# Kernel optimization log

Measured on AMD Instinct MI355X. Metric: run time of the kernel, lower is better.

The kernel has to match this reference:

```python
import jax, jax.numpy as jnp
import numpy as np
from jax import lax

_EPS = 1e-6
N_POINTS = 2048


def quat_to_rot(q):
    # q = (x, y, z, w), same convention as quaternion_to_rotation_matrix_torch
    # (its analytic Jacobians dR/dq in the kernel match this unnormalized form)
    x, y, z, w = q[0], q[1], q[2], q[3]
    return jnp.stack([
        jnp.stack([1 - 2 * (y * y + z * z), 2 * (x * y - z * w), 2 * (x * z + y * w)]),
        jnp.stack([2 * (x * y + z * w), 1 - 2 * (x * x + z * z), 2 * (y * z - x * w)]),
        jnp.stack([2 * (x * z - y * w), 2 * (y * z + x * w), 1 - 2 * (x * x + y * y)]),
    ])


def setup_inputs() -> dict:
    key = jax.random.key(0)
    ks = jax.random.split(key, 8)
    H, W = 512, 512
    # points in front of camera, projecting inside the image
    z = jax.random.uniform(ks[0], (N_POINTS, 1), minval=2.0, maxval=6.0)
    xy_dir = jax.random.uniform(ks[1], (N_POINTS, 2), minval=-0.45, maxval=0.45)
    pointcloud = jnp.concatenate([xy_dir * z, z], axis=1)  # [N,3]
    point_color = jax.random.uniform(ks[2], (N_POINTS, 3))
    point_alpha = jax.random.uniform(ks[3], (N_POINTS,), minval=0.1, maxval=0.9)
    # conic = inverse 2x2 covariance in pixel space, stored (a, b, c):
    ac = jax.random.uniform(ks[4], (N_POINTS, 2), minval=0.02, maxval=0.10)
    b = jax.random.uniform(ks[5], (N_POINTS, 1), minval=-0.01, maxval=0.01)
    point_conic = jnp.concatenate([ac[:, :1], b, ac[:, 1:]], axis=1)  # [N,3]
    # near-identity camera pose (x,y,z,w quaternion)
    q = jnp.array([0.01, -0.02, 0.015, 1.0], dtype=jnp.float32)
    q_pointcloud_camera = q / jnp.linalg.norm(q)
    t_pointcloud_camera = 0.05 * jax.random.normal(ks[6], (3,), dtype=jnp.float32)
    fx = fy = 500.0
    camera_intrinsics = jnp.array([[fx, 0.0, W / 2.0], [0.0, fy, H / 2.0], [0.0, 0.0, 1.0]], dtype=jnp.float32)
    return {
        "pointcloud": pointcloud.astype(jnp.float32),
        "point_color": point_color.astype(jnp.float32),
        "point_alpha": point_alpha.astype(jnp.float32),
        "point_conic": point_conic.astype(jnp.float32),
        "q_pointcloud_camera": q_pointcloud_camera,
        "t_pointcloud_camera": t_pointcloud_camera,
        "camera_intrinsics": camera_intrinsics,
        "camera_height": H,
        "camera_width": W,
    }


def _rasterize(pointcloud, point_color, point_alpha, point_conic, q, t, K, H, W):
    R = quat_to_rot(q)
    p_cam = pointcloud @ R.T + t  # [N,3] camera-frame positions
    depth = p_cam[:, 2]
    proj = p_cam @ K.T
    uv = proj[:, :2] / (depth[:, None] + _EPS)  # [N,2] pixel coords
    # depth sort (front-to-back), matching the sorted per-tile traversal
    order = jnp.argsort(depth)
    uv_s = uv[order]
    conic_s = point_conic[order]
    col_s = point_color[order]
    a_s = point_alpha[order]
    d_s = depth[order]

    px = jnp.arange(W, dtype=jnp.float32) + 0.5  # pixel centers, as in kernel
    py = jnp.arange(H, dtype=jnp.float32) + 0.5

    def step(carry, xs):
        T, rgb, dacc = carry
        uv_i, conic_i, col_i, a_i, d_i = xs
        dx = px[None, :] - uv_i[0]  # [1,W] -> broadcast [H,W]
        dy = py[:, None] - uv_i[1]  # [H,1]
        power = -0.5 * (conic_i[0] * dx * dx + 2.0 * conic_i[1] * dx * dy + conic_i[2] * dy * dy)
        g = jnp.exp(jnp.minimum(power, 0.0))  # gaussian density in [0,1]
        prod = g * a_i
        alpha = jnp.where(prod >= 1.0 / 255.0, jnp.minimum(prod, 0.99), 0.0)
        w = T * alpha
        rgb = rgb + w[..., None] * col_i
        dacc = dacc + w * d_i
        T = T * (1.0 - alpha)
        return (T, rgb, dacc), None

    carry0 = (jnp.ones((H, W), jnp.float32), jnp.zeros((H, W, 3), jnp.float32), jnp.zeros((H, W), jnp.float32))
    (T, rgb, dacc), _ = lax.scan(step, carry0, (uv_s, conic_s, col_s, a_s, d_s))
    # [H,W,5] = rgb, rasterized_depth, accumulated_alpha
    return jnp.concatenate([rgb, dacc[..., None], (1.0 - T)[..., None]], axis=-1)


def reference(pointcloud, point_color, point_alpha, point_conic, q_pointcloud_camera, t_pointcloud_camera, camera_intrinsics, camera_height, camera_width):
    return _rasterize(pointcloud, point_color, point_alpha, point_conic,
                      q_pointcloud_camera, t_pointcloud_camera, camera_intrinsics,
                      camera_height, camera_width)
```

## Files before the change

### kernel.cpp

```cpp
#include <hip/hip_runtime.h>
#include <math.h>

#define NPTS 2048
#define IMG_W 512
#define IMG_H 512
#define TILE 16
#define CAP 384
#define RSTRIDE 12

__global__ __launch_bounds__(256) void gs_fused(
    const float* __restrict__ pc,
    const float* __restrict__ col,
    const float* __restrict__ alp,
    const float* __restrict__ con,
    const float* __restrict__ q,
    const float* __restrict__ t,
    const float* __restrict__ K,
    float* __restrict__ out) {
  __shared__ float s_pts[CAP * RSTRIDE];
  __shared__ float2 s_do[CAP];
  __shared__ int s_cnt[32];

  int tid = threadIdx.x;
  int lane = tid & 63, wave = tid >> 6;
  int tilex = (blockIdx.x % (IMG_W / TILE)) * TILE;
  int tiley = (blockIdx.x / (IMG_W / TILE)) * TILE;
  int lx = tid % TILE, ly = tid / TILE;
  float px = tilex + lx + 0.5f, py = tiley + ly + 0.5f;
  float tx0 = tilex + 0.5f, tx1 = tilex + TILE - 0.5f;
  float ty0 = tiley + 0.5f, ty1 = tiley + TILE - 0.5f;

  float qx = q[0], qy = q[1], qz = q[2], qw = q[3];
  float r00 = 1.f - 2.f * (qy * qy + qz * qz), r01 = 2.f * (qx * qy - qz * qw),
        r02 = 2.f * (qx * qz + qy * qw);
  float r10 = 2.f * (qx * qy + qz * qw), r11 = 1.f - 2.f * (qx * qx + qz * qz),
        r12 = 2.f * (qy * qz - qx * qw);
  float r20 = 2.f * (qx * qz - qy * qw), r21 = 2.f * (qy * qz + qx * qw),
        r22 = 1.f - 2.f * (qx * qx + qy * qy);
  float t0 = t[0], t1 = t[1], t2 = t[2];
  float fx = K[0], cx = K[2], fy = K[4], cy = K[5];

#define PROJ(i, ux, uy, Z)                              \
  float ux, uy, Z;                                      \
  {                                                     \
    float x = pc[3 * (i)], y = pc[3 * (i) + 1],         \
          z = pc[3 * (i) + 2];                          \
    Z = r20 * x + r21 * y + r22 * z + t2;               \
    float X = r00 * x + r01 * y + r02 * z + t0;         \
    float Y = r10 * x + r11 * y + r12 * z + t1;         \
    float inv = 1.0f / (Z + 1e-6f);                     \
    ux = (fx * X + cx * Z) * inv;                       \
    uy = (fy * Y + cy * Z) * inv;                       \
  }

  unsigned pmask = 0;
  int miw[8];
#pragma unroll
  for (int c = 0; c < 8; c++) {
    int i = c * 256 + tid;
    PROJ(i, ux, uy, Z);
    float A = con[3 * i], B = con[3 * i + 1], C = con[3 * i + 2];
    float a = alp[i];
    float th = 2.0f * __logf(255.0f * a);
    float absB = fabsf(B);
    float dxm = fmaxf(0.0f, fmaxf(tx0 - ux, ux - tx1));
    float dym = fmaxf(0.0f, fmaxf(ty0 - uy, uy - ty1));
    float bound =
        fmaxf(A - absB, 0.0f) * dxm * dxm + fmaxf(C - absB, 0.0f) * dym * dym;
    bool pred = bound <= th + 1e-3f;
    unsigned long long m = __ballot(pred);
    miw[c] = __popcll(m & ((1ull << lane) - 1ull));
    if (lane == 0) s_cnt[c * 4 + wave] = (int)__popcll(m);
    pmask |= (unsigned)pred << c;
  }
  __syncthreads();

  int start[8], total;
  {
    int run = 0;
#pragma unroll
    for (int c = 0; c < 8; c++) {
      int s0 = s_cnt[c * 4 + 0], s1 = s_cnt[c * 4 + 1];
      int s2 = s_cnt[c * 4 + 2], s3 = s_cnt[c * 4 + 3];
      start[c] = run + (wave > 0 ? s0 : 0) + (wave > 1 ? s1 : 0) +
                 (wave > 2 ? s2 : 0);
      run += s0 + s1 + s2 + s3;
    }
    total = run;
  }

  float T = 1.0f, accr = 0.f, accg = 0.f, accb = 0.f, accd = 0.f;

#define COMPOSITE(w0, w1, w2)                                              \
  {                                                                        \
    float dx = px - w0.x, dy = py - w0.y;                                  \
    float pw =                                                             \
        -0.5f * (w0.z * dx * dx + 2.0f * w0.w * dx * dy + w1.x * dy * dy); \
    float gg = __expf(fminf(pw, 0.0f));                                    \
    float prod = gg * w1.y;                                                \
    if (prod >= (1.0f / 255.0f)) {                                         \
      float al = fminf(prod, 0.99f);                                       \
      float w = T * al;                                                    \
      accr += w * w2.x;                                                    \
      accg += w * w2.y;                                                    \
      accb += w * w2.z;                                                    \
      accd += w * w1.z;                                                    \
      T *= (1.0f - al);                                                    \
    }                                                                      \
  }

  if (total <= CAP) {
#pragma unroll
    for (int c = 0; c < 8; c++) {
      if ((pmask >> c) & 1) {
        int i = c * 256 + tid;
        PROJ(i, ux, uy, Z);
        float a = alp[i];
        int slot = start[c] + miw[c];
        float4* d = (float4*)(s_pts + (size_t)slot * RSTRIDE);
        d[0] = {ux, uy, con[3 * i], con[3 * i + 1]};
        d[1] = {con[3 * i + 2], a, Z, (float)i};
        d[2] = {col[3 * i], col[3 * i + 1], col[3 * i + 2], 0.0f};
        s_do[slot] = {Z, (float)i};
      }
    }
    __syncthreads();

    int k1 = tid, k2 = tid + 256;
    bool h1 = k1 < total, h2 = k2 < total;
    float2 d1 = h1 ? s_do[k1] : make_float2(1e30f, 1e30f);
    float2 d2 = h2 ? s_do[k2] : make_float2(1e30f, 1e30f);
    int r1 = 0, r2 = 0;
    for (int j = 0; j < total; j++) {
      float2 v = s_do[j];
      r1 += (v.x < d1.x) || (v.x == d1.x && v.y < d1.y);
      r2 += (v.x < d2.x) || (v.x == d2.x && v.y < d2.y);
    }
    float4 a1, b1, c1, a2, b2, c2;
    if (h1) {
      const float4* s = (const float4*)(s_pts + (size_t)k1 * RSTRIDE);
      a1 = s[0]; b1 = s[1]; c1 = s[2];
    }
    if (h2) {
      const float4* s = (const float4*)(s_pts + (size_t)k2 * RSTRIDE);
      a2 = s[0]; b2 = s[1]; c2 = s[2];
    }
    __syncthreads();
    if (h1) {
      float4* d = (float4*)(s_pts + (size_t)r1 * RSTRIDE);
      d[0] = a1; d[1] = b1; d[2] = c1;
    }
    if (h2) {
      float4* d = (float4*)(s_pts + (size_t)r2 * RSTRIDE);
      d[0] = a2; d[1] = b2; d[2] = c2;
    }
    __syncthreads();

    for (int k = 0; k < total; k++) {
      const float4* p4 = (const float4*)(s_pts + (size_t)k * RSTRIDE);
      float4 w0 = p4[0], w1 = p4[1], w2 = p4[2];
      COMPOSITE(w0, w1, w2);
      if (T < 1e-4f) break;
    }
  } else {
    float dep[8];
#pragma unroll
    for (int c = 0; c < 8; c++) {
      int i = c * 256 + tid;
      float x = pc[3 * i], y = pc[3 * i + 1], z = pc[3 * i + 2];
      dep[c] = r20 * x + r21 * y + r22 * z + t2;
    }
    unsigned live = pmask;
    float* s_rd = s_pts;
    int* s_ro = (int*)(s_pts + 256);
    float* s_rec = s_pts + 512;
    while (1) {
      float bd = 1e30f;
      int bo = 0x7fffffff;
#pragma unroll
      for (int c = 0; c < 8; c++) {
        if ((live >> c) & 1) {
          int o = c * 256 + tid;
          if (dep[c] < bd || (dep[c] == bd && o < bo)) { bd = dep[c]; bo = o; }
        }
      }
      s_rd[tid] = bd;
      s_ro[tid] = bo;
      __syncthreads();
      float wd = 1e30f;
      int wo = 0x7fffffff;
      for (int j = 0; j < 256; j++) {
        float d = s_rd[j];
        int o = s_ro[j];
        if (d < wd || (d == wd && o < wo)) { wd = d; wo = o; }
      }
      __syncthreads();
      if (wo == 0x7fffffff) break;
      if (tid == (wo & 255)) {
        int i = wo;
        PROJ(i, ux, uy, Z);
        float a = alp[i];
        float4* d = (float4*)s_rec;
        d[0] = {ux, uy, con[3 * i], con[3 * i + 1]};
        d[1] = {con[3 * i + 2], a, Z, (float)i};
        d[2] = {col[3 * i], col[3 * i + 1], col[3 * i + 2], 0.0f};
        live &= ~(1u << (wo >> 8));
      }
      __syncthreads();
      float4 w0 = ((float4*)s_rec)[0], w1 = ((float4*)s_rec)[1],
             w2 = ((float4*)s_rec)[2];
      COMPOSITE(w0, w1, w2);
    }
  }
#undef COMPOSITE
#undef PROJ

  int o = ((tiley + ly) * IMG_W + (tilex + lx)) * 5;
  out[o + 0] = accr;
  out[o + 1] = accg;
  out[o + 2] = accb;
  out[o + 3] = accd;
  out[o + 4] = 1.0f - T;
}

extern "C" void kernel_launch(void* const* d_in, const int* in_sizes, int n_in,
                              void* d_out, int out_size, void* d_ws,
                              size_t ws_size, hipStream_t stream) {
  const float* pc = (const float*)d_in[0];
  const float* col = (const float*)d_in[1];
  const float* alp = (const float*)d_in[2];
  const float* con = (const float*)d_in[3];
  const float* q = (const float*)d_in[4];
  const float* t = (const float*)d_in[5];
  const float* K = (const float*)d_in[6];
  float* out = (float*)d_out;

  gs_fused<<<(IMG_H / TILE) * (IMG_W / TILE), 256, 0, stream>>>(
      pc, col, alp, con, q, t, K, out);
}
```

Measured before the change: 20.80 us.

## Use 32x16 tiles with 512 threads and sort by index permutation

Grows each block to a 32x16 pixel tile with 512 threads, so there are half as many blocks and each loads the point list once for twice as many pixels. Sorting now ranks packed 64-bit (depth, index) keys, one per thread, and writes a permutation array instead of scattering the 48-byte records. Compositing reads records indirectly through that permutation. The early exit when transmittance drops below 1e-4 is removed, so every pixel walks the whole list, which can add compositing work.

Result: faster. 18.38 us (-11.6%).

```diff
diff --git a/kernel.cpp b/kernel.cpp
--- a/kernel.cpp
+++ b/kernel.cpp
@@ -4,11 +4,16 @@
 #define NPTS 2048
 #define IMG_W 512
 #define IMG_H 512
-#define TILE 16
-#define CAP 384
+#define RW 32
+#define RH 16
+#define NBX (IMG_W / RW)
+#define NBY (IMG_H / RH)
+#define NTHREADS (RW * RH)
+#define NCHUNK (NPTS / NTHREADS)
+#define CAP 512
 #define RSTRIDE 12
 
-__global__ __launch_bounds__(256) void gs_fused(
+__global__ __launch_bounds__(NTHREADS) void gs_fused(
     const float* __restrict__ pc,
     const float* __restrict__ col,
     const float* __restrict__ alp,
@@ -18,17 +23,18 @@
     const float* __restrict__ K,
     float* __restrict__ out) {
   __shared__ float s_pts[CAP * RSTRIDE];
-  __shared__ float2 s_do[CAP];
-  __shared__ int s_cnt[32];
+  __shared__ unsigned long long s_key[CAP];
+  __shared__ int s_order[CAP];
+  __shared__ int s_cnt[NCHUNK * 8];
 
   int tid = threadIdx.x;
   int lane = tid & 63, wave = tid >> 6;
-  int tilex = (blockIdx.x % (IMG_W / TILE)) * TILE;
-  int tiley = (blockIdx.x / (IMG_W / TILE)) * TILE;
-  int lx = tid % TILE, ly = tid / TILE;
-  float px = tilex + lx + 0.5f, py = tiley + ly + 0.5f;
-  float tx0 = tilex + 0.5f, tx1 = tilex + TILE - 0.5f;
-  float ty0 = tiley + 0.5f, ty1 = tiley + TILE - 0.5f;
+  int rx = (blockIdx.x % NBX) * RW;
+  int ry = (blockIdx.x / NBX) * RH;
+  int lx = tid % RW, ly = tid / RW;
+  float px = rx + lx + 0.5f, py = ry + ly + 0.5f;
+  float tx0 = rx + 0.5f, tx1 = rx + RW - 0.5f;
+  float ty0 = ry + 0.5f, ty1 = ry + RH - 0.5f;
 
   float qx = q[0], qy = q[1], qz = q[2], qw = q[3];
   float r00 = 1.f - 2.f * (qy * qy + qz * qz), r01 = 2.f * (qx * qy - qz * qw),
@@ -40,24 +46,24 @@
   float t0 = t[0], t1 = t[1], t2 = t[2];
   float fx = K[0], cx = K[2], fy = K[4], cy = K[5];
 
-#define PROJ(i, ux, uy, Z)                              \
-  float ux, uy, Z;                                      \
-  {                                                     \
-    float x = pc[3 * (i)], y = pc[3 * (i) + 1],         \
-          z = pc[3 * (i) + 2];                          \
-    Z = r20 * x + r21 * y + r22 * z + t2;               \
-    float X = r00 * x + r01 * y + r02 * z + t0;         \
-    float Y = r10 * x + r11 * y + r12 * z + t1;         \
-    float inv = 1.0f / (Z + 1e-6f);                     \
-    ux = (fx * X + cx * Z) * inv;                       \
-    uy = (fy * Y + cy * Z) * inv;                       \
+#define PROJ(i, ux, uy, Z)                      \
+  float ux, uy, Z;                              \
+  {                                             \
+    float x = pc[3 * (i)], y = pc[3 * (i) + 1], \
+          z = pc[3 * (i) + 2];                  \
+    Z = r20 * x + r21 * y + r22 * z + t2;       \
+    float X = r00 * x + r01 * y + r02 * z + t0; \
+    float Y = r10 * x + r11 * y + r12 * z + t1; \
+    float inv = 1.0f / (Z + 1e-6f);             \
+    ux = (fx * X + cx * Z) * inv;               \
+    uy = (fy * Y + cy * Z) * inv;               \
   }
 
   unsigned pmask = 0;
-  int miw[8];
-#pragma unroll
-  for (int c = 0; c < 8; c++) {
-    int i = c * 256 + tid;
+  int miw[NCHUNK];
+#pragma unroll
+  for (int c = 0; c < NCHUNK; c++) {
+    int i = c * NTHREADS + tid;
     PROJ(i, ux, uy, Z);
     float A = con[3 * i], B = con[3 * i + 1], C = con[3 * i + 2];
     float a = alp[i];
@@ -70,21 +76,25 @@
     bool pred = bound <= th + 1e-3f;
     unsigned long long m = __ballot(pred);
     miw[c] = __popcll(m & ((1ull << lane) - 1ull));
-    if (lane == 0) s_cnt[c * 4 + wave] = (int)__popcll(m);
+    if (lane == 0) s_cnt[c * 8 + wave] = (int)__popcll(m);
     pmask |= (unsigned)pred << c;
   }
   __syncthreads();
 
-  int start[8], total;
+  int start[NCHUNK], total;
   {
     int run = 0;
 #pragma unroll
-    for (int c = 0; c < 8; c++) {
-      int s0 = s_cnt[c * 4 + 0], s1 = s_cnt[c * 4 + 1];
-      int s2 = s_cnt[c * 4 + 2], s3 = s_cnt[c * 4 + 3];
-      start[c] = run + (wave > 0 ? s0 : 0) + (wave > 1 ? s1 : 0) +
-                 (wave > 2 ? s2 : 0);
-      run += s0 + s1 + s2 + s3;
+    for (int c = 0; c < NCHUNK; c++) {
+      int woff = 0, ct = 0;
+#pragma unroll
+      for (int w = 0; w < 8; w++) {
+        int v = s_cnt[c * 8 + w];
+        woff += (w < wave) ? v : 0;
+        ct += v;
+      }
+      start[c] = run + woff;
+      run += ct;
     }
     total = run;
   }
@@ -111,76 +121,56 @@
 
   if (total <= CAP) {
 #pragma unroll
-    for (int c = 0; c < 8; c++) {
+    for (int c = 0; c < NCHUNK; c++) {
       if ((pmask >> c) & 1) {
-        int i = c * 256 + tid;
+        int i = c * NTHREADS + tid;
         PROJ(i, ux, uy, Z);
         float a = alp[i];
+        float th = 2.0f * __logf(255.0f * a);
         int slot = start[c] + miw[c];
         float4* d = (float4*)(s_pts + (size_t)slot * RSTRIDE);
         d[0] = {ux, uy, con[3 * i], con[3 * i + 1]};
-        d[1] = {con[3 * i + 2], a, Z, (float)i};
+        d[1] = {con[3 * i + 2], a, Z, th};
         d[2] = {col[3 * i], col[3 * i + 1], col[3 * i + 2], 0.0f};
-        s_do[slot] = {Z, (float)i};
+        s_key[slot] =
+            ((unsigned long long)__float_as_uint(Z) << 32) | (unsigned)i;
       }
     }
     __syncthreads();
 
-    int k1 = tid, k2 = tid + 256;
-    bool h1 = k1 < total, h2 = k2 < total;
-    float2 d1 = h1 ? s_do[k1] : make_float2(1e30f, 1e30f);
-    float2 d2 = h2 ? s_do[k2] : make_float2(1e30f, 1e30f);
-    int r1 = 0, r2 = 0;
-    for (int j = 0; j < total; j++) {
-      float2 v = s_do[j];
-      r1 += (v.x < d1.x) || (v.x == d1.x && v.y < d1.y);
-      r2 += (v.x < d2.x) || (v.x == d2.x && v.y < d2.y);
-    }
-    float4 a1, b1, c1, a2, b2, c2;
-    if (h1) {
-      const float4* s = (const float4*)(s_pts + (size_t)k1 * RSTRIDE);
-      a1 = s[0]; b1 = s[1]; c1 = s[2];
-    }
-    if (h2) {
-      const float4* s = (const float4*)(s_pts + (size_t)k2 * RSTRIDE);
-      a2 = s[0]; b2 = s[1]; c2 = s[2];
+    if (tid < total) {
+      unsigned long long myk = s_key[tid];
+      int pos = 0;
+      for (int j = 0; j < total; j++) pos += (s_key[j] < myk);
+      s_order[pos] = tid;
     }
     __syncthreads();
-    if (h1) {
-      float4* d = (float4*)(s_pts + (size_t)r1 * RSTRIDE);
-      d[0] = a1; d[1] = b1; d[2] = c1;
-    }
-    if (h2) {
-      float4* d = (float4*)(s_pts + (size_t)r2 * RSTRIDE);
-      d[0] = a2; d[1] = b2; d[2] = c2;
-    }
-    __syncthreads();
-
-    for (int k = 0; k < total; k++) {
-      const float4* p4 = (const float4*)(s_pts + (size_t)k * RSTRIDE);
+
+    for (int kk = 0; kk < total; kk++) {
+      int e = s_order[kk];
+      const float4* p4 = (const float4*)(s_pts + (size_t)e * RSTRIDE);
       float4 w0 = p4[0], w1 = p4[1], w2 = p4[2];
       COMPOSITE(w0, w1, w2);
-      if (T < 1e-4f) break;
     }
   } else {
-    float dep[8];
-#pragma unroll
-    for (int c = 0; c < 8; c++) {
-      int i = c * 256 + tid;
+    float dep[NCHUNK];
+#pragma unroll
+    for (int c = 0; c < NCHUNK; c++) {
+      int i = c * NTHREADS + tid;
       float x = pc[3 * i], y = pc[3 * i + 1], z = pc[3 * i + 2];
       dep[c] = r20 * x + r21 * y + r22 * z + t2;
     }
     unsigned live = pmask;
     float* s_rd = s_pts;
-    int* s_ro = (int*)(s_pts + 256);
-    float* s_rec = s_pts + 512;
+    int* s_ro = (int*)(s_pts + NTHREADS);
+    float* s_rec = s_pts + 2 * NTHREADS;
     while (1) {
       float bd = 1e30f;
       int bo = 0x7fffffff;
 #pragma unroll
-      for (int c = 0; c < 8; c++) {
+      for (int c = 0; c < NCHUNK; c++) {
         if ((live >> c) & 1) {
-          int o = c * 256 + tid;
+          int o = c * NTHREADS + tid;
           if (dep[c] < bd || (dep[c] == bd && o < bo)) { bd = dep[c]; bo = o; }
         }
       }
@@ -189,22 +179,22 @@
       __syncthreads();
       float wd = 1e30f;
       int wo = 0x7fffffff;
-      for (int j = 0; j < 256; j++) {
+      for (int j = 0; j < NTHREADS; j++) {
         float d = s_rd[j];
         int o = s_ro[j];
         if (d < wd || (d == wd && o < wo)) { wd = d; wo = o; }
       }
       __syncthreads();
       if (wo == 0x7fffffff) break;
-      if (tid == (wo & 255)) {
+      if (tid == (wo & (NTHREADS - 1))) {
         int i = wo;
         PROJ(i, ux, uy, Z);
         float a = alp[i];
         float4* d = (float4*)s_rec;
         d[0] = {ux, uy, con[3 * i], con[3 * i + 1]};
-        d[1] = {con[3 * i + 2], a, Z, (float)i};
+        d[1] = {con[3 * i + 2], a, Z, 0.0f};
         d[2] = {col[3 * i], col[3 * i + 1], col[3 * i + 2], 0.0f};
-        live &= ~(1u << (wo >> 8));
+        live &= ~(1u << (wo / NTHREADS));
       }
       __syncthreads();
       float4 w0 = ((float4*)s_rec)[0], w1 = ((float4*)s_rec)[1],
@@ -215,7 +205,7 @@
 #undef COMPOSITE
 #undef PROJ
 
-  int o = ((tiley + ly) * IMG_W + (tilex + lx)) * 5;
+  int o = ((ry + ly) * IMG_W + (rx + lx)) * 5;
   out[o + 0] = accr;
   out[o + 1] = accg;
   out[o + 2] = accb;
@@ -235,6 +225,6 @@
   const float* K = (const float*)d_in[6];
   float* out = (float*)d_out;
 
-  gs_fused<<<(IMG_H / TILE) * (IMG_W / TILE), 256, 0, stream>>>(
-      pc, col, alp, con, q, t, K, out);
+  gs_fused<<<NBX * NBY, NTHREADS, 0, stream>>>(pc, col, alp, con, q, t, K,
+                                               out);
 }
```
